# Optimization experiments

Hardware: AMD Instinct MI355X
Metric: run time of the kernel (lower is better)

## Reference

```python
import jax, jax.numpy as jnp
import numpy as np


def _conv1x1(x, w, b=None):
    # x: (N,C,H,W), w: (O,C) -> (N,O,H,W)
    y = jnp.einsum('nchw,oc->nohw', x, w)
    return y if b is None else y + b[None, :, None, None]


def _norm(f):
    # per-channel zero-mean / unit-std over (N,H,W); torch.std is unbiased (ddof=1)
    mean = f.mean(axis=(0, 2, 3), keepdims=True)
    std = f.std(axis=(0, 2, 3), ddof=1, keepdims=True)
    return (f - mean) / (std + 1e-6)


def _causal_attention(x, w_cls):
    N, C, H, W = x.shape
    M = _conv1x1(x, w_cls).reshape(N, -1, H * W)     # (N,K,HW)
    sm = jax.nn.softmax(M, axis=2)                   # softmax over spatial
    return jnp.einsum('nkp,ncp->nkc', sm, x.reshape(N, C, H * W))  # (N,K,C)


def _ccnet(x, wq, bq, wk, bk, wv, bv, gamma1):
    B, C, H, W = x.shape
    q = _conv1x1(x, wq, bq)  # (B,Cq,H,W)
    k = _conv1x1(x, wk, bk)
    v = _conv1x1(x, wv, bv)  # (B,C,H,W)
    # column (vertical) attention energies with -inf on the self diagonal
    eH = jnp.einsum('bciw,bcjw->biwj', q, k)         # (B,H,W,H)
    eH = jnp.where(jnp.eye(H, dtype=bool)[None, :, None, :], -jnp.inf, eH)
    # row (horizontal) attention energies
    eW = jnp.einsum('bchi,bchj->bhij', q, k)         # (B,H,W,W)
    att = jax.nn.softmax(jnp.concatenate([eH, eW], axis=3), axis=3)
    attH, attW = att[..., :H], att[..., H:]
    outH = jnp.einsum('bcjw,biwj->bciw', v, attH)    # aggregate along column
    outW = jnp.einsum('bchj,bhij->bchi', v, attW)    # aggregate along row
    return gamma1 * (outH + outW) + x


def setup_inputs() -> dict:
    key = jax.random.key(0)
    ks = jax.random.split(key, 10)
    B, C, H, W = 8, 256, 96, 96
    Cq, K = C // 8, 6
    f32 = jnp.float32
    return {
        'preds_S': jax.random.normal(ks[0], (B, C, H, W), f32),
        'preds_T': jax.random.normal(ks[1], (B, C, H, W), f32),
        'w_cls': jax.random.normal(ks[2], (K, C), f32) * 0.05,
        'wq': jax.random.normal(ks[3], (Cq, C), f32) * 0.05,
        'bq': jnp.zeros((Cq,), f32),
        'wk': jax.random.normal(ks[4], (Cq, C), f32) * 0.05,
        'bk': jnp.zeros((Cq,), f32),
        'wv': jax.random.normal(ks[5], (C, C), f32) * 0.05,
        'bv': jnp.zeros((C,), f32),
        'gamma1': jax.random.normal(ks[6], (1,), f32) * 0.1,
    }


def reference(preds_S, preds_T, w_cls, wq, bq, wk, bk, wv, bv, gamma1):
    CA_W, CC_W = 0.0005, 1e-05
    N = preds_S.shape[0]
    s = _norm(preds_S)
    t = _norm(preds_T)
    ca_t = _causal_attention(t, w_cls)
    ca_s = _causal_attention(s, w_cls)
    ca_loss = jnp.sum((ca_t - ca_s) ** 2) / N
    cc_t = _ccnet(t, wq, bq, wk, bk, wv, bv, gamma1)
    cc_s = _ccnet(s, wq, bq, wk, bk, wv, bv, gamma1)
    cc_loss = jnp.sum((cc_t - cc_s) ** 2) / N
    return ca_loss * CA_W + cc_loss * CC_W
```

## Files before the change

kernel.cpp:

```cpp
#include <hip/hip_runtime.h>
#include <math.h>

#define NBAT 8
#define NC   256
#define NH   96
#define NW   96
#define NP   9216
#define NCQ  32
#define NKC  6
#define NL   192
#define NV   320
#define NTOT 73728

typedef __attribute__((ext_vector_type(4))) float  floatx4;
typedef __attribute__((ext_vector_type(8))) short  short8;

__device__ __forceinline__ float bf2f(unsigned short h){
  return __uint_as_float(((unsigned)h) << 16);
}
__device__ __forceinline__ float bflo(unsigned u){ return __uint_as_float(u << 16); }
__device__ __forceinline__ float bfhi(unsigned u){ return __uint_as_float(u & 0xFFFF0000u); }
__device__ __forceinline__ unsigned short f2bf(float f){
  unsigned u = __float_as_uint(f);
  u += 0x7FFFu + ((u >> 16) & 1u);
  return (unsigned short)(u >> 16);
}

union F4 { float4 v; float a[4]; };

__device__ __forceinline__ float warpReduceSum(float v){
  #pragma unroll
  for (int m = 32; m; m >>= 1) v += __shfl_xor(v, m);
  return v;
}
__device__ __forceinline__ float warpReduceMax(float v){
  #pragma unroll
  for (int m = 32; m; m >>= 1) v = fmaxf(v, __shfl_xor(v, m));
  return v;
}
__device__ float blockReduceSum(float v){
  __shared__ float lds[8];
  v = warpReduceSum(v);
  int wid = threadIdx.x >> 6, lane = threadIdx.x & 63;
  int nw = blockDim.x >> 6;
  if (lane == 0) lds[wid] = v;
  __syncthreads();
  if (wid == 0){
    v = (lane < nw) ? lds[lane] : 0.f;
    #pragma unroll
    for (int m = 4; m; m >>= 1) v += __shfl_xor(v, m);
  }
  __syncthreads();
  return v;
}
__device__ float blockReduceMax(float v){
  __shared__ float lds[8];
  v = warpReduceMax(v);
  int wid = threadIdx.x >> 6, lane = threadIdx.x & 63;
  int nw = blockDim.x >> 6;
  if (lane == 0) lds[wid] = v;
  __syncthreads();
  if (wid == 0){
    v = (lane < nw) ? lds[lane] : -INFINITY;
    #pragma unroll
    for (int m = 4; m; m >>= 1) v = fmaxf(v, __shfl_xor(v, m));
  }
  __syncthreads();
  return v;
}

__global__ __launch_bounds__(256)
void k_stats(const float* __restrict__ S, const float* __restrict__ T,
             float* __restrict__ s_sum, float* __restrict__ s_sq){
  int blk = blockIdx.x;
  int t = blk / (NC * NBAT);
  int rem = blk % (NC * NBAT);
  int c = rem / NBAT;
  int n = rem % NBAT;
  const float4* x4 = (const float4*)((t ? T : S) + ((size_t)n * NC + c) * NP);
  float s = 0.f, q = 0.f;
  for (int p = threadIdx.x; p < NP / 4; p += 256){
    F4 f; f.v = x4[p];
    #pragma unroll
    for (int j = 0; j < 4; j++){ s += f.a[j]; q += f.a[j] * f.a[j]; }
  }
  s = blockReduceSum(s);
  q = blockReduceSum(q);
  if (threadIdx.x == 0){
    atomicAdd(&s_sum[t * NC + c], s);
    atomicAdd(&s_sq[t * NC + c], q);
  }
}

__global__ __launch_bounds__(512)
void k_finalize(const float* __restrict__ s_sum, const float* __restrict__ s_sq,
                float* __restrict__ mean, float* __restrict__ inv){
  int i = threadIdx.x;
  if (i < 2 * NC){
    float s = s_sum[i], q = s_sq[i];
    float m = s / (float)NTOT;
    float var = (q - s * m) / (float)(NTOT - 1);
    var = fmaxf(var, 0.f);
    mean[i] = m;
    inv[i] = 1.f / (sqrtf(var) + 1e-6f);
  }
}

__global__ __launch_bounds__(256)
void k_caM(const float* __restrict__ S, const float* __restrict__ T,
           const float* __restrict__ wcls,
           const float* __restrict__ mean, const float* __restrict__ inv,
           float* __restrict__ smca){
  int pt = blockIdx.x, n = blockIdx.y, t = blockIdx.z;
  __shared__ float wsc[NKC * NC];
  __shared__ float shift[NKC];
  for (int idx = threadIdx.x; idx < NKC * NC; idx += 256){
    int c = idx & 255;
    wsc[idx] = wcls[idx] * inv[t * NC + c];
  }
  __syncthreads();
  if (threadIdx.x < NKC){
    float sh = 0.f;
    for (int c = 0; c < NC; c++) sh += wsc[threadIdx.x * NC + c] * mean[t * NC + c];
    shift[threadIdx.x] = sh;
  }
  __syncthreads();
  int p = pt * 256 + threadIdx.x;
  const float* x = (t ? T : S) + (size_t)n * NC * NP + p;
  float acc[NKC];
  #pragma unroll
  for (int k = 0; k < NKC; k++) acc[k] = 0.f;
  for (int c = 0; c < NC; c++){
    float xv = x[(size_t)c * NP];
    #pragma unroll
    for (int k = 0; k < NKC; k++) acc[k] += wsc[k * NC + c] * xv;
  }
  size_t base = ((size_t)(t * NBAT + n) * NKC) * NP + p;
  #pragma unroll
  for (int k = 0; k < NKC; k++) smca[base + (size_t)k * NP] = acc[k] - shift[k];
}

__global__ __launch_bounds__(256)
void k_caSoftmax(float* __restrict__ smca){
  int r = blockIdx.x;
  float* row = smca + (size_t)r * NP;
  float m = -INFINITY;
  for (int p = threadIdx.x; p < NP; p += 256) m = fmaxf(m, row[p]);
  m = blockReduceMax(m);
  __shared__ float bm, bs;
  if (threadIdx.x == 0) bm = m;
  __syncthreads();
  m = bm;
  float s = 0.f;
  for (int p = threadIdx.x; p < NP; p += 256) s += expf(row[p] - m);
  s = blockReduceSum(s);
  if (threadIdx.x == 0) bs = 1.f / s;
  __syncthreads();
  float rs = bs;
  for (int p = threadIdx.x; p < NP; p += 256) row[p] = expf(row[p] - m) * rs;
}

__global__ __launch_bounds__(256)
void k_caOut(const float* __restrict__ S, const float* __restrict__ T,
             const float* __restrict__ smca,
             const float* __restrict__ mean, const float* __restrict__ inv,
             float* __restrict__ ca){
  int ct = blockIdx.x & 7, ks = blockIdx.x >> 3;
  int n = blockIdx.y, t = blockIdx.z;
  int c0 = ct * 32;
  __shared__ float xt[32 * 264];
  __shared__ float smt[NKC * 256];
  int cl = threadIdx.x >> 3, pl = threadIdx.x & 7;
  float acc[NKC];
  #pragma unroll
  for (int k = 0; k < NKC; k++) acc[k] = 0.f;
  const float* xbase = (t ? T : S) + (size_t)n * NC * NP;
  const float* smbase = smca + (size_t)(t * NBAT + n) * NKC * NP;
  for (int pt = ks * 6; pt < ks * 6 + 6; pt++){
    int p0 = pt * 256;
    for (int idx = threadIdx.x; idx < 32 * 256; idx += 256){
      int r = idx >> 8, p = idx & 255;
      float v = xbase[(size_t)(c0 + r) * NP + p0 + p];
      xt[r * 264 + p] = (v - mean[t * NC + c0 + r]) * inv[t * NC + c0 + r];
    }
    for (int idx = threadIdx.x; idx < NKC * 256; idx += 256){
      int k = idx >> 8, p = idx & 255;
      smt[idx] = smbase[(size_t)k * NP + p0 + p];
    }
    __syncthreads();
    for (int j = 0; j < 32; j++){
      float xv = xt[cl * 264 + pl + 8 * j];
      #pragma unroll
      for (int k = 0; k < NKC; k++) acc[k] += smt[k * 256 + pl + 8 * j] * xv;
    }
    __syncthreads();
  }
  #pragma unroll
  for (int k = 0; k < NKC; k++){
    float v = acc[k];
    v += __shfl_xor(v, 1); v += __shfl_xor(v, 2); v += __shfl_xor(v, 4);
    if (pl == 0) atomicAdd(&ca[((size_t)(t * NBAT + n) * NKC + k) * NC + c0 + cl], v);
  }
}

__global__ __launch_bounds__(256)
void k_caLoss(const float* __restrict__ ca, float* __restrict__ out){
  int i = blockIdx.x * 256 + threadIdx.x;
  float d = 0.f;
  if (i < NBAT * NKC * NC) d = ca[(size_t)NBAT * NKC * NC + i] - ca[i];
  float ss = blockReduceSum(d * d);
  if (threadIdx.x == 0) atomicAdd(out, ss * (0.0005f / 8.0f));
}

__global__ __launch_bounds__(256)
void k_xn(const float* __restrict__ x0, int b0,
          const float* __restrict__ mean, const float* __restrict__ inv, int t,
          unsigned short* __restrict__ XN){
  int pt = blockIdx.x, ct = blockIdx.y, bb = blockIdx.z;
  int bg = b0 + bb;
  int p0 = pt * 64, c0 = ct * 64;
  __shared__ float tile[64 * 65];
  const float* x = x0 + ((size_t)bg * NC + c0) * NP + p0;
  #pragma unroll
  for (int i = 0; i < 4; i++){
    int idx = threadIdx.x + i * 256;
    int r = idx >> 4, g = (idx & 15) * 4;
    F4 f; f.v = *(const float4*)(x + (size_t)r * NP + g);
    float m = mean[t * NC + c0 + r], iv = inv[t * NC + c0 + r];
    #pragma unroll
    for (int j = 0; j < 4; j++) tile[(g + j) * 65 + r] = (f.a[j] - m) * iv;
  }
  __syncthreads();
  #pragma unroll
  for (int i = 0; i < 4; i++){
    int idx = threadIdx.x + i * 256;
    int p = idx >> 4, g = (idx & 15) * 4;
    unsigned lo = (unsigned)f2bf(tile[p * 65 + g + 0]) | ((unsigned)f2bf(tile[p * 65 + g + 1]) << 16);
    unsigned hi = (unsigned)f2bf(tile[p * 65 + g + 2]) | ((unsigned)f2bf(tile[p * 65 + g + 3]) << 16);
    uint2 u; u.x = lo; u.y = hi;
    *(uint2*)(XN + ((size_t)bb * NP + p0 + p) * NC + c0 + g) = u;
  }
}

__global__ __launch_bounds__(256)
void k_wconv(const float* __restrict__ wv, const float* __restrict__ wq,
             const float* __restrict__ wk, unsigned short* __restrict__ Wb){
  int n = blockIdx.x;
  const float* src = (n < 256) ? (wv + (size_t)n * NC)
                   : (n < 288) ? (wq + (size_t)(n - 256) * NC)
                               : (wk + (size_t)(n - 288) * NC);
  Wb[(size_t)n * NC + threadIdx.x] = f2bf(src[threadIdx.x]);
}

__global__ __launch_bounds__(256)
void k_v(const unsigned short* __restrict__ XN, const unsigned short* __restrict__ Wb,
         const float* __restrict__ bv, const float* __restrict__ bq,
         const float* __restrict__ bk,
         unsigned short* __restrict__ VT1,
         unsigned short* __restrict__ qb, unsigned short* __restrict__ kb){
  int pt = blockIdx.x, bb = blockIdx.y;
  int p0 = pt * 64;
  __shared__ unsigned short Wl[NV * 40];
  int lane = threadIdx.x & 63;
  int wid = threadIdx.x >> 6;
  int col = lane & 15, quad = lane >> 4;
  const unsigned short* xnb = XN + (size_t)bb * NP * NC + (size_t)(p0 + wid * 16 + col) * NC;
  floatx4 acc[20];
  #pragma unroll
  for (int nt = 0; nt < 20; nt++) acc[nt] = (floatx4){0.f, 0.f, 0.f, 0.f};

  int ci_n[5], ci_k8[5];
  #pragma unroll
  for (int i = 0; i < 5; i++){ int ci = i * 256 + threadIdx.x; ci_n[i] = ci >> 2; ci_k8[i] = (ci & 3) * 8; }

  short8 w[5];
  #pragma unroll
  for (int i = 0; i < 5; i++)
    w[i] = *(const short8*)(Wb + (size_t)ci_n[i] * NC + ci_k8[i]);

  for (int ks = 0; ks < 8; ks++){
    if (ks) __syncthreads();
    #pragma unroll
    for (int i = 0; i < 5; i++)
      *(short8*)(Wl + ci_n[i] * 40 + ci_k8[i]) = w[i];
    __syncthreads();
    if (ks < 7){
      int k0n = (ks + 1) * 32;
      #pragma unroll
      for (int i = 0; i < 5; i++)
        w[i] = *(const short8*)(Wb + (size_t)ci_n[i] * NC + k0n + ci_k8[i]);
    }
    short8 a = *(const short8*)(xnb + ks * 32 + quad * 8);
    #pragma unroll
    for (int nt = 0; nt < 20; nt++){
      short8 b = *(const short8*)(Wl + (nt * 16 + col) * 40 + quad * 8);
      acc[nt] = __builtin_amdgcn_mfma_f32_16x16x32_bf16(a, b, acc[nt], 0, 0, 0);
    }
  }

  int prow0 = p0 + wid * 16 + quad * 4;
  #pragma unroll
  for (int nt = 0; nt < 16; nt++){
    int c = nt * 16 + col;
    float bias = bv[c];
    uint2 u;
    u.x = (unsigned)f2bf(acc[nt][0] + bias) | ((unsigned)f2bf(acc[nt][1] + bias) << 16);
    u.y = (unsigned)f2bf(acc[nt][2] + bias) | ((unsigned)f2bf(acc[nt][3] + bias) << 16);
    *(uint2*)(VT1 + ((size_t)bb * NC + c) * NP + prow0) = u;
  }
  #pragma unroll
  for (int nt = 16; nt < 18; nt++){
    int c = (nt - 16) * 16 + col;
    float bias = bq[c];
    #pragma unroll
    for (int i = 0; i < 4; i++)
      qb[((size_t)bb * NP + prow0 + i) * NCQ + c] = f2bf(acc[nt][i] + bias);
  }
  #pragma unroll
  for (int nt = 18; nt < 20; nt++){
    int c = (nt - 18) * 16 + col;
    float bias = bk[c];
    #pragma unroll
    for (int i = 0; i < 4; i++)
      kb[((size_t)bb * NP + prow0 + i) * NCQ + c] = f2bf(acc[nt][i] + bias);
  }
}

__global__ __launch_bounds__(256)
void k_vt(const unsigned short* __restrict__ VT1, unsigned short* __restrict__ VT2){
  int c = blockIdx.x, bb = blockIdx.y;
  __shared__ unsigned short tile[96 * 104];
  size_t base = ((size_t)bb * NC + c) * NP;
  for (int idx = threadIdx.x; idx < 1152; idx += 256){
    int h = idx / 12, g = idx % 12;
    short8 v = *(const short8*)(VT1 + base + h * 96 + g * 8);
    #pragma unroll
    for (int kk = 0; kk < 8; kk++) tile[(g * 8 + kk) * 104 + h] = ((unsigned short*)&v)[kk];
  }
  __syncthreads();
  for (int idx = threadIdx.x; idx < 1152; idx += 256){
    int w = idx / 12, g = idx % 12;
    short8 v = *(const short8*)(tile + w * 104 + g * 8);
    *(short8*)(VT2 + base + w * 96 + g * 8) = v;
  }
}

__global__ __launch_bounds__(256)
void k_eH(const unsigned short* __restrict__ qb, const unsigned short* __restrict__ kb,
          unsigned short* __restrict__ att){
  int w = blockIdx.x, bb = blockIdx.y;
  int lane = threadIdx.x & 63, wid = threadIdx.x >> 6;
  int col = lane & 15, quad = lane >> 4;
  int mi0 = (wid & 1) * 3, ni0 = (wid >> 1) * 3;
  short8 a[3], b[3];
  #pragma unroll
  for (int m = 0; m < 3; m++)
    a[m] = *(const short8*)(qb + ((size_t)bb * NP + ((mi0 + m) * 16 + col) * 96 + w) * NCQ + quad * 8);
  #pragma unroll
  for (int n = 0; n < 3; n++)
    b[n] = *(const short8*)(kb + ((size_t)bb * NP + ((ni0 + n) * 16 + col) * 96 + w) * NCQ + quad * 8);
  floatx4 acc[3][3];
  #pragma unroll
  for (int m = 0; m < 3; m++)
    #pragma unroll
    for (int n = 0; n < 3; n++){
      acc[m][n] = (floatx4){0.f, 0.f, 0.f, 0.f};
      acc[m][n] = __builtin_amdgcn_mfma_f32_16x16x32_bf16(a[m], b[n], acc[m][n], 0, 0, 0);
    }
  #pragma unroll
  for (int m = 0; m < 3; m++)
    #pragma unroll
    for (int n = 0; n < 3; n++){
      int j = (ni0 + n) * 16 + col;
      #pragma unroll
      for (int r = 0; r < 4; r++){
        int i = (mi0 + m) * 16 + quad * 4 + r;
        float v = (j == i) ? -INFINITY : acc[m][n][r];
        att[((size_t)bb * NP + i * 96 + w) * NL + j] = f2bf(v);
      }
    }
}

__global__ __launch_bounds__(256)
void k_eW(const unsigned short* __restrict__ qb, const unsigned short* __restrict__ kb,
          unsigned short* __restrict__ att){
  int h = blockIdx.x, bb = blockIdx.y;
  int lane = threadIdx.x & 63, wid = threadIdx.x >> 6;
  int col = lane & 15, quad = lane >> 4;
  int mi0 = (wid & 1) * 3, ni0 = (wid >> 1) * 3;
  short8 a[3], b[3];
  #pragma unroll
  for (int m = 0; m < 3; m++)
    a[m] = *(const short8*)(qb + ((size_t)bb * NP + h * 96 + (mi0 + m) * 16 + col) * NCQ + quad * 8);
  #pragma unroll
  for (int n = 0; n < 3; n++)
    b[n] = *(const short8*)(kb + ((size_t)bb * NP + h * 96 + (ni0 + n) * 16 + col) * NCQ + quad * 8);
  floatx4 acc[3][3];
  #pragma unroll
  for (int m = 0; m < 3; m++)
    #pragma unroll
    for (int n = 0; n < 3; n++){
      acc[m][n] = (floatx4){0.f, 0.f, 0.f, 0.f};
      acc[m][n] = __builtin_amdgcn_mfma_f32_16x16x32_bf16(a[m], b[n], acc[m][n], 0, 0, 0);
    }
  #pragma unroll
  for (int m = 0; m < 3; m++)
    #pragma unroll
    for (int n = 0; n < 3; n++){
      int j = (ni0 + n) * 16 + col;
      #pragma unroll
      for (int r = 0; r < 4; r++){
        int i = (mi0 + m) * 16 + quad * 4 + r;
        att[((size_t)bb * NP + h * 96 + i) * NL + 96 + j] = f2bf(acc[m][n][r]);
      }
    }
}

__global__ __launch_bounds__(256)
void k_attSoftmax(unsigned short* __restrict__ att){
  int q = blockIdx.x * 4 + (threadIdx.x >> 6);
  int lane = threadIdx.x & 63;
  unsigned short* row = att + (size_t)q * NL;
  float e0 = bf2f(row[lane]);
  float e1 = bf2f(row[64 + lane]);
  float e2 = bf2f(row[128 + lane]);
  float m = fmaxf(e0, fmaxf(e1, e2));
  m = warpReduceMax(m);
  float x0 = expf(e0 - m), x1 = expf(e1 - m), x2 = expf(e2 - m);
  float s = warpReduceSum(x0 + x1 + x2);
  float rs = 1.f / s;
  row[lane]       = f2bf(x0 * rs);
  row[64 + lane]  = f2bf(x1 * rs);
  row[128 + lane] = f2bf(x2 * rs);
}

__global__ __launch_bounds__(256)
void k_outH(const unsigned short* __restrict__ VT2, const unsigned short* __restrict__ att,
            unsigned short* __restrict__ OH){
  int w = blockIdx.x, bb = blockIdx.y;
  int lane = threadIdx.x & 63, wid = threadIdx.x >> 6;
  int col = lane & 15, quad = lane >> 4;
  floatx4 acc[6][4];
  #pragma unroll
  for (int m = 0; m < 6; m++)
    #pragma unroll
    for (int n = 0; n < 4; n++) acc[m][n] = (floatx4){0.f, 0.f, 0.f, 0.f};
  #pragma unroll
  for (int ks = 0; ks < 3; ks++){
    int k0 = ks * 32 + quad * 8;
    short8 a[6], b[4];
    #pragma unroll
    for (int m = 0; m < 6; m++)
      a[m] = *(const short8*)(att + ((size_t)bb * NP + (m * 16 + col) * 96 + w) * NL + k0);
    #pragma unroll
    for (int n = 0; n < 4; n++){
      int c = wid * 64 + n * 16 + col;
      b[n] = *(const short8*)(VT2 + ((size_t)bb * NC + c) * NP + w * 96 + k0);
    }
    #pragma unroll
    for (int m = 0; m < 6; m++)
      #pragma unroll
      for (int n = 0; n < 4; n++)
        acc[m][n] = __builtin_amdgcn_mfma_f32_16x16x32_bf16(a[m], b[n], acc[m][n], 0, 0, 0);
  }
  #pragma unroll
  for (int m = 0; m < 6; m++)
    #pragma unroll
    for (int n = 0; n < 4; n++){
      int c = wid * 64 + n * 16 + col;
      #pragma unroll
      for (int r = 0; r < 4; r++){
        int i = m * 16 + quad * 4 + r;
        OH[((size_t)bb * NP + i * 96 + w) * NC + c] = f2bf(acc[m][n][r]);
      }
    }
}

__global__ __launch_bounds__(256)
void k_outW(const unsigned short* __restrict__ VT1, const unsigned short* __restrict__ att,
            const unsigned short* __restrict__ OH, unsigned short* __restrict__ Ot,
            const float* __restrict__ predsS, const float* __restrict__ predsT,
            const float* __restrict__ mean, const float* __restrict__ inv,
            const float* __restrict__ gamma, int b0, int spass,
            float* __restrict__ out){
  int h = blockIdx.x, bb = blockIdx.y;
  int lane = threadIdx.x & 63, wid = threadIdx.x >> 6;
  int col = lane & 15, quad = lane >> 4;
  floatx4 acc[6][4];
  #pragma unroll
  for (int m = 0; m < 6; m++)
    #pragma unroll
    for (int n = 0; n < 4; n++) acc[m][n] = (floatx4){0.f, 0.f, 0.f, 0.f};
  #pragma unroll
  for (int ks = 0; ks < 3; ks++){
    int k0 = ks * 32 + quad * 8;
    short8 a[6], b[4];
    #pragma unroll
    for (int m = 0; m < 6; m++)
      a[m] = *(const short8*)(att + ((size_t)bb * NP + h * 96 + m * 16 + col) * NL + 96 + k0);
    #pragma unroll
    for (int n = 0; n < 4; n++){
      int c = wid * 64 + n * 16 + col;
      b[n] = *(const short8*)(VT1 + ((size_t)bb * NC + c) * NP + h * 96 + k0);
    }
    #pragma unroll
    for (int m = 0; m < 6; m++)
      #pragma unroll
      for (int n = 0; n < 4; n++)
        acc[m][n] = __builtin_amdgcn_mfma_f32_16x16x32_bf16(a[m], b[n], acc[m][n], 0, 0, 0);
  }
  if (!spass){
    #pragma unroll
    for (int m = 0; m < 6; m++)
      #pragma unroll
      for (int n = 0; n < 4; n++){
        int c = wid * 64 + n * 16 + col;
        #pragma unroll
        for (int r = 0; r < 4; r++){
          int i = m * 16 + quad * 4 + r;
          size_t base = ((size_t)bb * NP + h * 96 + i) * NC + c;
          Ot[base] = f2bf(acc[m][n][r] + bf2f(OH[base]));
        }
      }
  } else {
    int bg = b0 + bb;
    float g = gamma[0];
    float ss = 0.f;
    #pragma unroll
    for (int n = 0; n < 4; n++){
      int c = wid * 64 + n * 16 + col;
      float mS = mean[c],      iS = inv[c];
      float mT = mean[NC + c], iT = inv[NC + c];
      const float* tp = predsT + ((size_t)bg * NC + c) * NP + h * 96;
      const float* sp = predsS + ((size_t)bg * NC + c) * NP + h * 96;
      #pragma unroll
      for (int m = 0; m < 6; m++){
        int i0 = m * 16 + quad * 4;
        F4 tv, sv;
        tv.v = *(const float4*)(tp + i0);
        sv.v = *(const float4*)(sp + i0);
        #pragma unroll
        for (int r = 0; r < 4; r++){
          size_t base = ((size_t)bb * NP + h * 96 + i0 + r) * NC + c;
          float os = acc[m][n][r] + bf2f(OH[base]);
          float ot = bf2f(Ot[base]);
          float dn = (tv.a[r] - mT) * iT - (sv.a[r] - mS) * iS;
          float d = g * (ot - os) + dn;
          ss += d * d;
        }
      }
    }
    ss = blockReduceSum(ss);
    if (threadIdx.x == 0) atomicAdd(out, ss * (1e-5f / 8.0f));
  }
}

extern "C" void kernel_launch(void* const* d_in, const int* in_sizes, int n_in,
                              void* d_out, int out_size, void* d_ws, size_t ws_size,
                              hipStream_t stream){
  (void)in_sizes; (void)n_in; (void)out_size;
  const float* S    = (const float*)d_in[0];
  const float* T    = (const float*)d_in[1];
  const float* wcls = (const float*)d_in[2];
  const float* wq   = (const float*)d_in[3];
  const float* bq   = (const float*)d_in[4];
  const float* wk   = (const float*)d_in[5];
  const float* bk   = (const float*)d_in[6];
  const float* wv   = (const float*)d_in[7];
  const float* bv   = (const float*)d_in[8];
  const float* gamma= (const float*)d_in[9];
  float* out = (float*)d_out;

  char* base = (char*)d_ws;
  size_t off = 0;
  auto alloc = [&](size_t b){ size_t o = off; off += (b + 255) & ~(size_t)255; return o; };
  size_t o_ssum = alloc(2 * NC * 4);
  size_t o_ssq  = alloc(2 * NC * 4);
  size_t o_mean = alloc(2 * NC * 4);
  size_t o_inv  = alloc(2 * NC * 4);
  size_t o_wb   = alloc((size_t)NV * NC * 2);
  size_t o_ca   = alloc((size_t)2 * NBAT * NKC * NC * 4);
  size_t o_smca = alloc((size_t)2 * NBAT * NKC * NP * 4);
  size_t fixed = off;
  size_t per_b = (size_t)NP * NC * 2 * 5
               + (size_t)NP * NCQ * 2 * 2
               + (size_t)NP * NL * 2;
  int NB = 8;
  while (NB > 1 && fixed + (size_t)NB * per_b + 8192 > ws_size) NB >>= 1;

  size_t o_xn  = alloc((size_t)NB * NP * NC * 2);
  size_t o_v1  = alloc((size_t)NB * NP * NC * 2);
  size_t o_v2  = alloc((size_t)NB * NP * NC * 2);
  size_t o_q   = alloc((size_t)NB * NP * NCQ * 2);
  size_t o_k   = alloc((size_t)NB * NP * NCQ * 2);
  size_t o_att = alloc((size_t)NB * NP * NL * 2);
  size_t o_oh  = alloc((size_t)NB * NP * NC * 2);
  size_t o_ot  = alloc((size_t)NB * NP * NC * 2);

  float* ssum = (float*)(base + o_ssum);
  float* ssq  = (float*)(base + o_ssq);
  float* mean = (float*)(base + o_mean);
  float* inv  = (float*)(base + o_inv);
  float* ca   = (float*)(base + o_ca);
  float* smca = (float*)(base + o_smca);
  unsigned short* Wb  = (unsigned short*)(base + o_wb);
  unsigned short* XN  = (unsigned short*)(base + o_xn);
  unsigned short* VT1 = (unsigned short*)(base + o_v1);
  unsigned short* VT2 = (unsigned short*)(base + o_v2);
  unsigned short* qbp = (unsigned short*)(base + o_q);
  unsigned short* kbp = (unsigned short*)(base + o_k);
  unsigned short* att = (unsigned short*)(base + o_att);
  unsigned short* OH  = (unsigned short*)(base + o_oh);
  unsigned short* Ot  = (unsigned short*)(base + o_ot);

  hipMemsetAsync(d_out, 0, 4, stream);
  hipMemsetAsync(base + o_ssum, 0, 4096, stream);
  hipMemsetAsync(base + o_ca, 0, (size_t)2 * NBAT * NKC * NC * 4, stream);

  k_stats<<<dim3(2 * NC * NBAT), 256, 0, stream>>>(S, T, ssum, ssq);
  k_finalize<<<1, 512, 0, stream>>>(ssum, ssq, mean, inv);
  k_wconv<<<dim3(NV), 256, 0, stream>>>(wv, wq, wk, Wb);

  k_caM<<<dim3(36, NBAT, 2), 256, 0, stream>>>(S, T, wcls, mean, inv, smca);
  k_caSoftmax<<<dim3(2 * NBAT * NKC), 256, 0, stream>>>(smca);
  k_caOut<<<dim3(48, NBAT, 2), 256, 0, stream>>>(S, T, smca, mean, inv, ca);
  k_caLoss<<<dim3(48), 256, 0, stream>>>(ca, out);

  for (int b0 = 0; b0 < NBAT; b0 += NB){
    for (int pass = 0; pass < 2; pass++){
      int t = (pass == 0) ? 1 : 0;
      const float* x = t ? T : S;
      k_xn<<<dim3(144, 4, NB), 256, 0, stream>>>(x, b0, mean, inv, t, XN);
      k_v<<<dim3(144, NB), 256, 0, stream>>>(XN, Wb, bv, bq, bk, VT1, qbp, kbp);
      k_vt<<<dim3(NC, NB), 256, 0, stream>>>(VT1, VT2);
      k_eH<<<dim3(96, NB), 256, 0, stream>>>(qbp, kbp, att);
      k_eW<<<dim3(96, NB), 256, 0, stream>>>(qbp, kbp, att);
      k_attSoftmax<<<dim3(NB * 2304), 256, 0, stream>>>(att);
      k_outH<<<dim3(96, NB), 256, 0, stream>>>(VT2, att, OH);
      k_outW<<<dim3(96, NB), 256, 0, stream>>>(VT1, att, OH, Ot, S, T, mean, inv,
                                               gamma, b0, pass, out);
    }
  }
}
```

Baseline: 649.4 us.

## Compute causal-attention branch from the bf16 normalized tensor and vectorize outH/outW stores

The causal-attention logits and pooled outputs are now computed from the already-built bf16 channel-last normalized tensor inside the per-batch loop, instead of rereading the fp32 inputs twice. This removes two full passes over the large fp32 inputs. The outH/outW MFMA operands are swapped so each lane writes four contiguous channels as a packed uint2 store. The final loss epilogue now reads the residual from the bf16 tensor rather than renormalizing the fp32 inputs, which adds bf16 rounding to both the residual and the attention pooling.

Result: slower. 696.9 us (+7.3%).

```diff
diff --git a/kernel.cpp b/kernel.cpp
--- a/kernel.cpp
+++ b/kernel.cpp
@@ -107,37 +107,67 @@
 }
 
 __global__ __launch_bounds__(256)
-void k_caM(const float* __restrict__ S, const float* __restrict__ T,
-           const float* __restrict__ wcls,
-           const float* __restrict__ mean, const float* __restrict__ inv,
-           float* __restrict__ smca){
-  int pt = blockIdx.x, n = blockIdx.y, t = blockIdx.z;
-  __shared__ float wsc[NKC * NC];
-  __shared__ float shift[NKC];
-  for (int idx = threadIdx.x; idx < NKC * NC; idx += 256){
-    int c = idx & 255;
-    wsc[idx] = wcls[idx] * inv[t * NC + c];
-  }
-  __syncthreads();
-  if (threadIdx.x < NKC){
-    float sh = 0.f;
-    for (int c = 0; c < NC; c++) sh += wsc[threadIdx.x * NC + c] * mean[t * NC + c];
-    shift[threadIdx.x] = sh;
-  }
+void k_xn(const float* __restrict__ x0, int b0,
+          const float* __restrict__ mean, const float* __restrict__ inv, int t,
+          unsigned short* __restrict__ XN){
+  int pt = blockIdx.x, ct = blockIdx.y, bb = blockIdx.z;
+  int bg = b0 + bb;
+  int p0 = pt * 64, c0 = ct * 64;
+  __shared__ float tile[64 * 65];
+  const float* x = x0 + ((size_t)bg * NC + c0) * NP + p0;
+  #pragma unroll
+  for (int i = 0; i < 4; i++){
+    int idx = threadIdx.x + i * 256;
+    int r = idx >> 4, g = (idx & 15) * 4;
+    F4 f; f.v = *(const float4*)(x + (size_t)r * NP + g);
+    float m = mean[t * NC + c0 + r], iv = inv[t * NC + c0 + r];
+    #pragma unroll
+    for (int j = 0; j < 4; j++) tile[(g + j) * 65 + r] = (f.a[j] - m) * iv;
+  }
+  __syncthreads();
+  #pragma unroll
+  for (int i = 0; i < 4; i++){
+    int idx = threadIdx.x + i * 256;
+    int p = idx >> 4, g = (idx & 15) * 4;
+    unsigned lo = (unsigned)f2bf(tile[p * 65 + g + 0]) | ((unsigned)f2bf(tile[p * 65 + g + 1]) << 16);
+    unsigned hi = (unsigned)f2bf(tile[p * 65 + g + 2]) | ((unsigned)f2bf(tile[p * 65 + g + 3]) << 16);
+    uint2 u; u.x = lo; u.y = hi;
+    *(uint2*)(XN + ((size_t)bb * NP + p0 + p) * NC + c0 + g) = u;
+  }
+}
+
+__global__ __launch_bounds__(256)
+void k_wconv(const float* __restrict__ wv, const float* __restrict__ wq,
+             const float* __restrict__ wk, unsigned short* __restrict__ Wb){
+  int n = blockIdx.x;
+  const float* src = (n < 256) ? (wv + (size_t)n * NC)
+                   : (n < 288) ? (wq + (size_t)(n - 256) * NC)
+                               : (wk + (size_t)(n - 288) * NC);
+  Wb[(size_t)n * NC + threadIdx.x] = f2bf(src[threadIdx.x]);
+}
+
+__global__ __launch_bounds__(256)
+void k_caMB(const unsigned short* __restrict__ XN, const float* __restrict__ wcls,
+            float* __restrict__ smca){
+  int pt = blockIdx.x, bb = blockIdx.y;
+  __shared__ float wl[NKC * NC];
+  for (int idx = threadIdx.x; idx < NKC * NC; idx += 256) wl[idx] = wcls[idx];
   __syncthreads();
   int p = pt * 256 + threadIdx.x;
-  const float* x = (t ? T : S) + (size_t)n * NC * NP + p;
-  float acc[NKC];
-  #pragma unroll
-  for (int k = 0; k < NKC; k++) acc[k] = 0.f;
-  for (int c = 0; c < NC; c++){
-    float xv = x[(size_t)c * NP];
-    #pragma unroll
-    for (int k = 0; k < NKC; k++) acc[k] += wsc[k * NC + c] * xv;
-  }
-  size_t base = ((size_t)(t * NBAT + n) * NKC) * NP + p;
-  #pragma unroll
-  for (int k = 0; k < NKC; k++) smca[base + (size_t)k * NP] = acc[k] - shift[k];
+  const unsigned short* xr = XN + ((size_t)bb * NP + p) * NC;
+  float acc[NKC] = {};
+  for (int g = 0; g < 32; g++){
+    short8 x8 = *(const short8*)(xr + g * 8);
+    #pragma unroll
+    for (int e = 0; e < 8; e++){
+      float xv = bf2f(((unsigned short*)&x8)[e]);
+      int c = g * 8 + e;
+      #pragma unroll
+      for (int k = 0; k < NKC; k++) acc[k] += wl[k * NC + c] * xv;
+    }
+  }
+  #pragma unroll
+  for (int k = 0; k < NKC; k++) smca[((size_t)bb * NKC + k) * NP + p] = acc[k];
 }
 
 __global__ __launch_bounds__(256)
@@ -161,46 +191,45 @@
 }
 
 __global__ __launch_bounds__(256)
-void k_caOut(const float* __restrict__ S, const float* __restrict__ T,
-             const float* __restrict__ smca,
-             const float* __restrict__ mean, const float* __restrict__ inv,
-             float* __restrict__ ca){
-  int ct = blockIdx.x & 7, ks = blockIdx.x >> 3;
-  int n = blockIdx.y, t = blockIdx.z;
-  int c0 = ct * 32;
-  __shared__ float xt[32 * 264];
-  __shared__ float smt[NKC * 256];
-  int cl = threadIdx.x >> 3, pl = threadIdx.x & 7;
-  float acc[NKC];
-  #pragma unroll
-  for (int k = 0; k < NKC; k++) acc[k] = 0.f;
-  const float* xbase = (t ? T : S) + (size_t)n * NC * NP;
-  const float* smbase = smca + (size_t)(t * NBAT + n) * NKC * NP;
-  for (int pt = ks * 6; pt < ks * 6 + 6; pt++){
-    int p0 = pt * 256;
-    for (int idx = threadIdx.x; idx < 32 * 256; idx += 256){
-      int r = idx >> 8, p = idx & 255;
-      float v = xbase[(size_t)(c0 + r) * NP + p0 + p];
-      xt[r * 264 + p] = (v - mean[t * NC + c0 + r]) * inv[t * NC + c0 + r];
-    }
-    for (int idx = threadIdx.x; idx < NKC * 256; idx += 256){
-      int k = idx >> 8, p = idx & 255;
-      smt[idx] = smbase[(size_t)k * NP + p0 + p];
-    }
-    __syncthreads();
-    for (int j = 0; j < 32; j++){
-      float xv = xt[cl * 264 + pl + 8 * j];
-      #pragma unroll
-      for (int k = 0; k < NKC; k++) acc[k] += smt[k * 256 + pl + 8 * j] * xv;
-    }
-    __syncthreads();
-  }
-  #pragma unroll
-  for (int k = 0; k < NKC; k++){
-    float v = acc[k];
-    v += __shfl_xor(v, 1); v += __shfl_xor(v, 2); v += __shfl_xor(v, 4);
-    if (pl == 0) atomicAdd(&ca[((size_t)(t * NBAT + n) * NKC + k) * NC + c0 + cl], v);
-  }
+void k_caOutB(const unsigned short* __restrict__ XN, const float* __restrict__ smca,
+              float* __restrict__ ca, int t, int b0){
+  int ks = blockIdx.x, bb = blockIdx.y;
+  __shared__ float sml[NKC * 1152];
+  __shared__ float lca[NKC * NC];
+  int p0 = ks * 1152;
+  const float* smb = smca + (size_t)bb * NKC * NP;
+  for (int idx = threadIdx.x; idx < NKC * 1152; idx += 256){
+    int k = idx / 1152, pp = idx % 1152;
+    sml[idx] = smb[(size_t)k * NP + p0 + pp];
+  }
+  for (int idx = threadIdx.x; idx < NKC * NC; idx += 256) lca[idx] = 0.f;
+  __syncthreads();
+  int c8 = (threadIdx.x & 31) * 8, psub = threadIdx.x >> 5;
+  const unsigned short* xb = XN + (size_t)bb * NP * NC;
+  float acc[NKC][8] = {};
+  for (int j = 0; j < 144; j++){
+    int pp = psub + 8 * j;
+    short8 x8 = *(const short8*)(xb + (size_t)(p0 + pp) * NC + c8);
+    float xf[8];
+    #pragma unroll
+    for (int e = 0; e < 8; e++) xf[e] = bf2f(((unsigned short*)&x8)[e]);
+    #pragma unroll
+    for (int k = 0; k < NKC; k++){
+      float sv = sml[k * 1152 + pp];
+      #pragma unroll
+      for (int e = 0; e < 8; e++) acc[k][e] += sv * xf[e];
+    }
+  }
+  #pragma unroll
+  for (int k = 0; k < NKC; k++)
+    #pragma unroll
+    for (int e = 0; e < 8; e++) atomicAdd(&lca[k * NC + c8 + e], acc[k][e]);
+  __syncthreads();
+  int n = b0 + bb;
+  #pragma unroll
+  for (int k = 0; k < NKC; k++)
+    atomicAdd(&ca[((size_t)(t * NBAT + n) * NKC + k) * NC + threadIdx.x],
+              lca[k * NC + threadIdx.x]);
 }
 
 __global__ __launch_bounds__(256)
@@ -210,46 +239,6 @@
   if (i < NBAT * NKC * NC) d = ca[(size_t)NBAT * NKC * NC + i] - ca[i];
   float ss = blockReduceSum(d * d);
   if (threadIdx.x == 0) atomicAdd(out, ss * (0.0005f / 8.0f));
-}
-
-__global__ __launch_bounds__(256)
-void k_xn(const float* __restrict__ x0, int b0,
-          const float* __restrict__ mean, const float* __restrict__ inv, int t,
-          unsigned short* __restrict__ XN){
-  int pt = blockIdx.x, ct = blockIdx.y, bb = blockIdx.z;
-  int bg = b0 + bb;
-  int p0 = pt * 64, c0 = ct * 64;
-  __shared__ float tile[64 * 65];
-  const float* x = x0 + ((size_t)bg * NC + c0) * NP + p0;
-  #pragma unroll
-  for (int i = 0; i < 4; i++){
-    int idx = threadIdx.x + i * 256;
-    int r = idx >> 4, g = (idx & 15) * 4;
-    F4 f; f.v = *(const float4*)(x + (size_t)r * NP + g);
-    float m = mean[t * NC + c0 + r], iv = inv[t * NC + c0 + r];
-    #pragma unroll
-    for (int j = 0; j < 4; j++) tile[(g + j) * 65 + r] = (f.a[j] - m) * iv;
-  }
-  __syncthreads();
-  #pragma unroll
-  for (int i = 0; i < 4; i++){
-    int idx = threadIdx.x + i * 256;
-    int p = idx >> 4, g = (idx & 15) * 4;
-    unsigned lo = (unsigned)f2bf(tile[p * 65 + g + 0]) | ((unsigned)f2bf(tile[p * 65 + g + 1]) << 16);
-    unsigned hi = (unsigned)f2bf(tile[p * 65 + g + 2]) | ((unsigned)f2bf(tile[p * 65 + g + 3]) << 16);
-    uint2 u; u.x = lo; u.y = hi;
-    *(uint2*)(XN + ((size_t)bb * NP + p0 + p) * NC + c0 + g) = u;
-  }
-}
-
-__global__ __launch_bounds__(256)
-void k_wconv(const float* __restrict__ wv, const float* __restrict__ wq,
-             const float* __restrict__ wk, unsigned short* __restrict__ Wb){
-  int n = blockIdx.x;
-  const float* src = (n < 256) ? (wv + (size_t)n * NC)
-                   : (n < 288) ? (wq + (size_t)(n - 256) * NC)
-                               : (wk + (size_t)(n - 288) * NC);
-  Wb[(size_t)n * NC + threadIdx.x] = f2bf(src[threadIdx.x]);
 }
 
 __global__ __launch_bounds__(256)
@@ -440,116 +429,116 @@
   int w = blockIdx.x, bb = blockIdx.y;
   int lane = threadIdx.x & 63, wid = threadIdx.x >> 6;
   int col = lane & 15, quad = lane >> 4;
-  floatx4 acc[6][4];
-  #pragma unroll
-  for (int m = 0; m < 6; m++)
-    #pragma unroll
-    for (int n = 0; n < 4; n++) acc[m][n] = (floatx4){0.f, 0.f, 0.f, 0.f};
+  floatx4 acc[4][6];
+  #pragma unroll
+  for (int ct = 0; ct < 4; ct++)
+    #pragma unroll
+    for (int it = 0; it < 6; it++) acc[ct][it] = (floatx4){0.f, 0.f, 0.f, 0.f};
   #pragma unroll
   for (int ks = 0; ks < 3; ks++){
     int k0 = ks * 32 + quad * 8;
-    short8 a[6], b[4];
-    #pragma unroll
-    for (int m = 0; m < 6; m++)
-      a[m] = *(const short8*)(att + ((size_t)bb * NP + (m * 16 + col) * 96 + w) * NL + k0);
-    #pragma unroll
-    for (int n = 0; n < 4; n++){
-      int c = wid * 64 + n * 16 + col;
-      b[n] = *(const short8*)(VT2 + ((size_t)bb * NC + c) * NP + w * 96 + k0);
-    }
-    #pragma unroll
-    for (int m = 0; m < 6; m++)
-      #pragma unroll
-      for (int n = 0; n < 4; n++)
-        acc[m][n] = __builtin_amdgcn_mfma_f32_16x16x32_bf16(a[m], b[n], acc[m][n], 0, 0, 0);
-  }
-  #pragma unroll
-  for (int m = 0; m < 6; m++)
-    #pragma unroll
-    for (int n = 0; n < 4; n++){
-      int c = wid * 64 + n * 16 + col;
-      #pragma unroll
-      for (int r = 0; r < 4; r++){
-        int i = m * 16 + quad * 4 + r;
-        OH[((size_t)bb * NP + i * 96 + w) * NC + c] = f2bf(acc[m][n][r]);
-      }
+    short8 a[4], b[6];
+    #pragma unroll
+    for (int ct = 0; ct < 4; ct++){
+      int c = wid * 64 + ct * 16 + col;
+      a[ct] = *(const short8*)(VT2 + ((size_t)bb * NC + c) * NP + w * 96 + k0);
+    }
+    #pragma unroll
+    for (int it = 0; it < 6; it++){
+      int i = it * 16 + col;
+      b[it] = *(const short8*)(att + ((size_t)bb * NP + i * 96 + w) * NL + k0);
+    }
+    #pragma unroll
+    for (int ct = 0; ct < 4; ct++)
+      #pragma unroll
+      for (int it = 0; it < 6; it++)
+        acc[ct][it] = __builtin_amdgcn_mfma_f32_16x16x32_bf16(a[ct], b[it], acc[ct][it], 0, 0, 0);
+  }
+  #pragma unroll
+  for (int ct = 0; ct < 4; ct++)
+    #pragma unroll
+    for (int it = 0; it < 6; it++){
+      int c0 = wid * 64 + ct * 16 + quad * 4;
+      int i = it * 16 + col;
+      uint2 u;
+      u.x = (unsigned)f2bf(acc[ct][it][0]) | ((unsigned)f2bf(acc[ct][it][1]) << 16);
+      u.y = (unsigned)f2bf(acc[ct][it][2]) | ((unsigned)f2bf(acc[ct][it][3]) << 16);
+      *(uint2*)(OH + ((size_t)bb * NP + i * 96 + w) * NC + c0) = u;
     }
 }
 
 __global__ __launch_bounds__(256)
 void k_outW(const unsigned short* __restrict__ VT1, const unsigned short* __restrict__ att,
-            const unsigned short* __restrict__ OH, unsigned short* __restrict__ Ot,
-            const float* __restrict__ predsS, const float* __restrict__ predsT,
-            const float* __restrict__ mean, const float* __restrict__ inv,
-            const float* __restrict__ gamma, int b0, int spass,
+            const unsigned short* __restrict__ OH, unsigned short* __restrict__ OtL,
+            const unsigned short* __restrict__ XN,
+            const float* __restrict__ gamma, int spass,
             float* __restrict__ out){
   int h = blockIdx.x, bb = blockIdx.y;
   int lane = threadIdx.x & 63, wid = threadIdx.x >> 6;
   int col = lane & 15, quad = lane >> 4;
-  floatx4 acc[6][4];
-  #pragma unroll
-  for (int m = 0; m < 6; m++)
-    #pragma unroll
-    for (int n = 0; n < 4; n++) acc[m][n] = (floatx4){0.f, 0.f, 0.f, 0.f};
+  float g = gamma[0];
+  floatx4 acc[4][6];
+  #pragma unroll
+  for (int ct = 0; ct < 4; ct++)
+    #pragma unroll
+    for (int it = 0; it < 6; it++) acc[ct][it] = (floatx4){0.f, 0.f, 0.f, 0.f};
   #pragma unroll
   for (int ks = 0; ks < 3; ks++){
     int k0 = ks * 32 + quad * 8;
-    short8 a[6], b[4];
-    #pragma unroll
-    for (int m = 0; m < 6; m++)
-      a[m] = *(const short8*)(att + ((size_t)bb * NP + h * 96 + m * 16 + col) * NL + 96 + k0);
-    #pragma unroll
-    for (int n = 0; n < 4; n++){
-      int c = wid * 64 + n * 16 + col;
-      b[n] = *(const short8*)(VT1 + ((size_t)bb * NC + c) * NP + h * 96 + k0);
-    }
-    #pragma unroll
-    for (int m = 0; m < 6; m++)
-      #pragma unroll
-      for (int n = 0; n < 4; n++)
-        acc[m][n] = __builtin_amdgcn_mfma_f32_16x16x32_bf16(a[m], b[n], acc[m][n], 0, 0, 0);
+    short8 a[4], b[6];
+    #pragma unroll
+    for (int ct = 0; ct < 4; ct++){
+      int c = wid * 64 + ct * 16 + col;
+      a[ct] = *(const short8*)(VT1 + ((size_t)bb * NC + c) * NP + h * 96 + k0);
+    }
+    #pragma unroll
+    for (int it = 0; it < 6; it++){
+      int i = it * 16 + col;
+      b[it] = *(const short8*)(att + ((size_t)bb * NP + h * 96 + i) * NL + 96 + k0);
+    }
+    #pragma unroll
+    for (int ct = 0; ct < 4; ct++)
+      #pragma unroll
+      for (int it = 0; it < 6; it++)
+        acc[ct][it] = __builtin_amdgcn_mfma_f32_16x16x32_bf16(a[ct], b[it], acc[ct][it], 0, 0, 0);
   }
   if (!spass){
     #pragma unroll
-    for (int m = 0; m < 6; m++)
-      #pragma unroll
-      for (int n = 0; n < 4; n++){
-        int c = wid * 64 + n * 16 + col;
-        #pragma unroll
-        for (int r = 0; r < 4; r++){
-          int i = m * 16 + quad * 4 + r;
-          size_t base = ((size_t)bb * NP + h * 96 + i) * NC + c;
-          Ot[base] = f2bf(acc[m][n][r] + bf2f(OH[base]));
-        }
+    for (int ct = 0; ct < 4; ct++)
+      #pragma unroll
+      for (int it = 0; it < 6; it++){
+        int c0 = wid * 64 + ct * 16 + quad * 4;
+        int i = it * 16 + col;
+        size_t base = ((size_t)bb * NP + h * 96 + i) * NC + c0;
+        uint2 uoh = *(const uint2*)(OH + base);
+        uint2 uxn = *(const uint2*)(XN + base);
+        float o0 = g * (acc[ct][it][0] + bflo(uoh.x)) + bflo(uxn.x);
+        float o1 = g * (acc[ct][it][1] + bfhi(uoh.x)) + bfhi(uxn.x);
+        float o2 = g * (acc[ct][it][2] + bflo(uoh.y)) + bflo(uxn.y);
+        float o3 = g * (acc[ct][it][3] + bfhi(uoh.y)) + bfhi(uxn.y);
+        uint2 u;
+        u.x = (unsigned)f2bf(o0) | ((unsigned)f2bf(o1) << 16);
+        u.y = (unsigned)f2bf(o2) | ((unsigned)f2bf(o3) << 16);
+        *(uint2*)(OtL + base) = u;
       }
   } else {
-    int bg = b0 + bb;
-    float g = gamma[0];
     float ss = 0.f;
     #pragma unroll
-    for (int n = 0; n < 4; n++){
-      int c = wid * 64 + n * 16 + col;
-      float mS = mean[c],      iS = inv[c];
-      float mT = mean[NC + c], iT = inv[NC + c];
-      const float* tp = predsT + ((size_t)bg * NC + c) * NP + h * 96;
-      const float* sp = predsS + ((size_t)bg * NC + c) * NP + h * 96;
-      #pragma unroll
-      for (int m = 0; m < 6; m++){
-        int i0 = m * 16 + quad * 4;
-        F4 tv, sv;
-        tv.v = *(const float4*)(tp + i0);
-        sv.v = *(const float4*)(sp + i0);
-        #pragma unroll
-        for (int r = 0; r < 4; r++){
-          size_t base = ((size_t)bb * NP + h * 96 + i0 + r) * NC + c;
-          float os = acc[m][n][r] + bf2f(OH[base]);
-          float ot = bf2f(Ot[base]);
-          float dn = (tv.a[r] - mT) * iT - (sv.a[r] - mS) * iS;
-          float d = g * (ot - os) + dn;
-          ss += d * d;
-        }
+    for (int ct = 0; ct < 4; ct++)
+      #pragma unroll
+      for (int it = 0; it < 6; it++){
+        int c0 = wid * 64 + ct * 16 + quad * 4;
+        int i = it * 16 + col;
+        size_t base = ((size_t)bb * NP + h * 96 + i) * NC + c0;
+        uint2 uoh = *(const uint2*)(OH + base);
+        uint2 uxn = *(const uint2*)(XN + base);
+        uint2 uot = *(const uint2*)(OtL + base);
+        float d0 = bflo(uot.x) - (g * (acc[ct][it][0] + bflo(uoh.x)) + bflo(uxn.x));
+        float d1 = bfhi(uot.x) - (g * (acc[ct][it][1] + bfhi(uoh.x)) + bfhi(uxn.x));
+        float d2 = bflo(uot.y) - (g * (acc[ct][it][2] + bflo(uoh.y)) + bflo(uxn.y));
+        float d3 = bfhi(uot.y) - (g * (acc[ct][it][3] + bfhi(uoh.y)) + bfhi(uxn.y));
+        ss += d0 * d0 + d1 * d1 + d2 * d2 + d3 * d3;
       }
-    }
     ss = blockReduceSum(ss);
     if (threadIdx.x == 0) atomicAdd(out, ss * (1e-5f / 8.0f));
   }
@@ -580,11 +569,11 @@
   size_t o_inv  = alloc(2 * NC * 4);
   size_t o_wb   = alloc((size_t)NV * NC * 2);
   size_t o_ca   = alloc((size_t)2 * NBAT * NKC * NC * 4);
-  size_t o_smca = alloc((size_t)2 * NBAT * NKC * NP * 4);
   size_t fixed = off;
   size_t per_b = (size_t)NP * NC * 2 * 5
                + (size_t)NP * NCQ * 2 * 2
-               + (size_t)NP * NL * 2;
+               + (size_t)NP * NL * 2
+               + (size_t)NKC * NP * 4;
   int NB = 8;
   while (NB > 1 && fixed + (size_t)NB * per_b + 8192 > ws_size) NB >>= 1;
 
@@ -596,13 +585,14 @@
   size_t o_att = alloc((size_t)NB * NP * NL * 2);
   size_t o_oh  = alloc((size_t)NB * NP * NC * 2);
   size_t o_ot  = alloc((size_t)NB * NP * NC * 2);
+  size_t o_sm  = alloc((size_t)NB * NKC * NP * 4);
 
   float* ssum = (float*)(base + o_ssum);
   float* ssq  = (float*)(base + o_ssq);
   float* mean = (float*)(base + o_mean);
   float* inv  = (float*)(base + o_inv);
   float* ca   = (float*)(base + o_ca);
-  float* smca = (float*)(base + o_smca);
+  float* smca = (float*)(base + o_sm);
   unsigned short* Wb  = (unsigned short*)(base + o_wb);
   unsigned short* XN  = (unsigned short*)(base + o_xn);
   unsigned short* VT1 = (unsigned short*)(base + o_v1);
@@ -611,7 +601,7 @@
   unsigned short* kbp = (unsigned short*)(base + o_k);
   unsigned short* att = (unsigned short*)(base + o_att);
   unsigned short* OH  = (unsigned short*)(base + o_oh);
-  unsigned short* Ot  = (unsigned short*)(base + o_ot);
+  unsigned short* OtL = (unsigned short*)(base + o_ot);
 
   hipMemsetAsync(d_out, 0, 4, stream);
   hipMemsetAsync(base + o_ssum, 0, 4096, stream);
@@ -620,25 +610,24 @@
   k_stats<<<dim3(2 * NC * NBAT), 256, 0, stream>>>(S, T, ssum, ssq);
   k_finalize<<<1, 512, 0, stream>>>(ssum, ssq, mean, inv);
   k_wconv<<<dim3(NV), 256, 0, stream>>>(wv, wq, wk, Wb);
-
-  k_caM<<<dim3(36, NBAT, 2), 256, 0, stream>>>(S, T, wcls, mean, inv, smca);
-  k_caSoftmax<<<dim3(2 * NBAT * NKC), 256, 0, stream>>>(smca);
-  k_caOut<<<dim3(48, NBAT, 2), 256, 0, stream>>>(S, T, smca, mean, inv, ca);
-  k_caLoss<<<dim3(48), 256, 0, stream>>>(ca, out);
 
   for (int b0 = 0; b0 < NBAT; b0 += NB){
     for (int pass = 0; pass < 2; pass++){
       int t = (pass == 0) ? 1 : 0;
       const float* x = t ? T : S;
       k_xn<<<dim3(144, 4, NB), 256, 0, stream>>>(x, b0, mean, inv, t, XN);
+      k_caMB<<<dim3(36, NB), 256, 0, stream>>>(XN, wcls, smca);
+      k_caSoftmax<<<dim3(NB * NKC), 256, 0, stream>>>(smca);
+      k_caOutB<<<dim3(8, NB), 256, 0, stream>>>(XN, smca, ca, t, b0);
       k_v<<<dim3(144, NB), 256, 0, stream>>>(XN, Wb, bv, bq, bk, VT1, qbp, kbp);
       k_vt<<<dim3(NC, NB), 256, 0, stream>>>(VT1, VT2);
       k_eH<<<dim3(96, NB), 256, 0, stream>>>(qbp, kbp, att);
       k_eW<<<dim3(96, NB), 256, 0, stream>>>(qbp, kbp, att);
       k_attSoftmax<<<dim3(NB * 2304), 256, 0, stream>>>(att);
       k_outH<<<dim3(96, NB), 256, 0, stream>>>(VT2, att, OH);
-      k_outW<<<dim3(96, NB), 256, 0, stream>>>(VT1, att, OH, Ot, S, T, mean, inv,
-                                               gamma, b0, pass, out);
-    }
-  }
-}
+      k_outW<<<dim3(96, NB), 256, 0, stream>>>(VT1, att, OH, OtL, XN,
+                                               gamma, pass, out);
+    }
+  }
+  k_caLoss<<<dim3(48), 256, 0, stream>>>(ca, out);
+}
```
